# Optimization experiments

Measured on AMD Instinct MI355X. Metric: run time of the kernel, lower is better.

Reference implementation:

```python
import jax, jax.numpy as jnp
import numpy as np

B, H, S, D = 4, 16, 2048, 64

def setup_inputs() -> dict:
    key = jax.random.key(0)
    kq, kk, kv = jax.random.split(key, 3)
    q = jax.random.normal(kq, (B, H, S, D), dtype=jnp.float32)
    k = jax.random.normal(kk, (B, H, S, D), dtype=jnp.float32)
    v = jax.random.normal(kv, (B, H, S, D), dtype=jnp.float32)
    return {"q": q, "k": k, "v": v}

def reference(q, k, v):
    # dots: [b,h,i,j] = q . k (NO 1/sqrt(d) scaling, matching source)
    dots = jnp.einsum('bhid,bhjd->bhij', q, k)
    # causal=False (and the source's causal mask is a no-op bug anyway)
    attn = jax.nn.softmax(dots, axis=-1)
    # out: [b,h,i,d] = sum_j attn[b,h,i,j] * v[b,h,j,d]
    return jnp.einsum('bhjd,bhij->bhid', v, attn)
```

## Files before the change

### kernel.cpp

```cpp
#include <hip/hip_runtime.h>
#include <hip/hip_bf16.h>
#include <stdint.h>

#define B_ 4
#define H_ 16
#define S_ 2048
#define D_ 64
#define QBLK 128
#define KBLK 64
#define LDW 72

typedef __attribute__((ext_vector_type(8))) short short8;
typedef __attribute__((ext_vector_type(4))) float f32x4;
typedef __attribute__((ext_vector_type(16))) float f32x16;
typedef _Float16 f16x8 __attribute__((ext_vector_type(8)));
typedef _Float16 f16x4 __attribute__((ext_vector_type(4)));
typedef __fp16 fp16x2 __attribute__((ext_vector_type(2)));

__device__ __forceinline__ unsigned short f2bf(float f) {
  union { float f; unsigned int u; } x; x.f = f;
  unsigned int u = x.u;
  unsigned int r = (u + 0x7FFFu + ((u >> 16) & 1u)) >> 16;
  return (unsigned short)r;
}
__device__ __forceinline__ float bf2f(unsigned short h) {
  union { unsigned int u; float f; } y; y.u = ((unsigned int)h) << 16;
  return y.f;
}

__device__ __forceinline__ unsigned pkrtz(float a, float b) {
  union { fp16x2 h; unsigned u; } c;
  c.h = __builtin_amdgcn_cvt_pkrtz(a, b);
  return c.u;
}

__device__ __forceinline__ void swap32(unsigned &a, unsigned &b) {
#if __has_builtin(__builtin_amdgcn_permlane32_swap)
  typedef int i32x2 __attribute__((ext_vector_type(2)));
  i32x2 r = __builtin_amdgcn_permlane32_swap((int)a, (int)b, false, false);
  a = (unsigned)r[0]; b = (unsigned)r[1];
#else
  unsigned pa = (unsigned)__shfl_xor((int)a, 32);
  unsigned pb = (unsigned)__shfl_xor((int)b, 32);
  bool lo = (threadIdx.x & 32) == 0;
  unsigned r0 = lo ? a : pb;
  unsigned r1 = lo ? pa : b;
  a = r0; b = r1;
#endif
}

#define GLOAD16(g, l) __builtin_amdgcn_global_load_lds( \
    (const __attribute__((address_space(1))) unsigned int*)(g), \
    (__attribute__((address_space(3))) unsigned int*)(l), 16, 0, 0)

__global__ void prep_k(const float* __restrict__ K, _Float16* __restrict__ Kp) {
  int e4 = (blockIdx.x * 256 + threadIdx.x) * 4;
  int bh  = e4 >> 17;
  int rem = e4 & 131071;
  int s   = rem >> 6;
  int d0  = rem & 63;
  const float4 kv = *(const float4*)(K + (size_t)e4);
  f16x4 h;
  h[0] = (_Float16)kv.x; h[1] = (_Float16)kv.y;
  h[2] = (_Float16)kv.z; h[3] = (_Float16)kv.w;
  size_t off = ((size_t)bh * S_ + s) * 128 + (unsigned)((d0 * 2) ^ ((s & 7) << 4));
  *(f16x4*)((char*)Kp + off) = h;
}

__global__ void prep_v(const float* __restrict__ V, _Float16* __restrict__ Vt) {
  __shared__ _Float16 tile[64][68];
  int bh = blockIdx.x >> 5;
  int st = blockIdx.x & 31;
  const float* Vb = V + ((size_t)bh * S_ + st * 64) * 64;
  int tid = threadIdx.x;
  #pragma unroll
  for (int i = 0; i < 4; ++i) {
    int idx = i * 1024 + tid * 4;
    int r = idx >> 6, c = idx & 63;
    float4 vv = *(const float4*)(Vb + (size_t)r * 64 + c);
    f16x4 o;
    o[0] = (_Float16)vv.x; o[1] = (_Float16)vv.y;
    o[2] = (_Float16)vv.z; o[3] = (_Float16)vv.w;
    *(f16x4*)&tile[r][c] = o;
  }
  __syncthreads();
  int chunk = tid & 15;
  int dbase = tid >> 4;
  size_t outb = (size_t)bh * (64 * S_ * 2) + (size_t)st * 128;
  #pragma unroll
  for (int i = 0; i < 4; ++i) {
    int d = dbase + i * 16;
    f16x4 o;
    o[0] = tile[chunk * 4 + 0][d];
    o[1] = tile[chunk * 4 + 1][d];
    o[2] = tile[chunk * 4 + 2][d];
    o[3] = tile[chunk * 4 + 3][d];
    size_t off = outb + (size_t)d * (S_ * 2) + (unsigned)((chunk * 8) ^ ((d & 7) << 4));
    *(f16x4*)((char*)Vt + off) = o;
  }
}

__global__ __launch_bounds__(256)
void attn_fwd4(const float* __restrict__ Q, const _Float16* __restrict__ Kg,
               const _Float16* __restrict__ Vg, float* __restrict__ O) {
  __shared__ char smem[32768];

  const int tid  = threadIdx.x;
  const int lane = tid & 63;
  const int wid  = tid >> 6;
  const int l31  = lane & 31;
  const int hi   = lane >> 5;

  const int qtile = blockIdx.x;
  const int bh    = blockIdx.y;

  const char* KB = (const char*)Kg + (size_t)bh * (S_ * 128);
  const char* VB = (const char*)Vg + (size_t)bh * (64 * S_ * 2);
  const float* Qb = Q + (size_t)bh * S_ * D_;
  float*       Ob = O + (size_t)bh * S_ * D_;

  const int qrow = qtile * QBLK + wid * 32 + l31;
  f16x8 qf[4];
  #pragma unroll
  for (int ds = 0; ds < 4; ++ds) {
    const float* qp = Qb + (size_t)qrow * D_ + ds * 16 + hi * 8;
    float4 a = *(const float4*)(qp);
    float4 b = *(const float4*)(qp + 4);
    qf[ds][0] = (_Float16)a.x; qf[ds][1] = (_Float16)a.y;
    qf[ds][2] = (_Float16)a.z; qf[ds][3] = (_Float16)a.w;
    qf[ds][4] = (_Float16)b.x; qf[ds][5] = (_Float16)b.y;
    qf[ds][6] = (_Float16)b.z; qf[ds][7] = (_Float16)b.w;
  }

  f32x16 oacc[2];
  #pragma unroll
  for (int dn = 0; dn < 2; ++dn)
    #pragma unroll
    for (int r = 0; r < 16; ++r) oacc[dn][r] = 0.f;
  float m_r = -INFINITY, l_r = 0.f;

  #define STAGE(buf, kb)                                                        \
    {                                                                           \
      char* Kl_ = smem + (buf) * 16384;                                         \
      char* Vl_ = Kl_ + 8192;                                                   \
      _Pragma("unroll")                                                         \
      for (int c = 0; c < 4; ++c) {                                             \
        int id = c * 4 + wid;                                                   \
        if (id < 8) {                                                           \
          GLOAD16(KB + (size_t)(kb) * 128 + id * 1024 + lane * 16,              \
                  Kl_ + id * 1024);                                             \
        } else {                                                                \
          int i = id - 8;                                                       \
          GLOAD16(VB + (size_t)(i * 8 + (lane >> 3)) * (S_ * 2)                 \
                     + ((kb) >> 6) * 128 + (lane & 7) * 16,                     \
                  Vl_ + i * 1024);                                              \
        }                                                                       \
      }                                                                         \
    }

  STAGE(0, 0);
  __syncthreads();

  for (int it = 0; it < S_ / KBLK; ++it) {
    const int cur = it & 1;
    if (it < S_ / KBLK - 1) STAGE(cur ^ 1, (it + 1) * KBLK);

    const char* Kl = smem + cur * 16384;
    const char* Vl = Kl + 8192;

    f32x16 sacc[2];
    #pragma unroll
    for (int b = 0; b < 2; ++b) {
      #pragma unroll
      for (int r = 0; r < 16; ++r) sacc[b][r] = 0.f;
      const int row = b * 32 + l31;
      #pragma unroll
      for (int ds = 0; ds < 4; ++ds) {
        f16x8 kf = *(const f16x8*)(Kl + row * 128 + ((ds * 32 + hi * 16) ^ ((row & 7) << 4)));
        sacc[b] = __builtin_amdgcn_mfma_f32_32x32x16_f16(kf, qf[ds], sacc[b], 0, 0, 0);
      }
    }

    float t[16];
    #pragma unroll
    for (int r = 0; r < 16; ++r) t[r] = fmaxf(sacc[0][r], sacc[1][r]);
    #pragma unroll
    for (int s = 8; s > 0; s >>= 1)
      #pragma unroll
      for (int r = 0; r < 8; ++r)
        if (r < s) t[r] = fmaxf(t[r], t[r + s]);
    float mx = fmaxf(t[0], __shfl_xor(t[0], 32));
    float nm = fmaxf(m_r, mx);
    float sc = __expf(m_r - nm);
    m_r = nm;

    float rs0 = 0.f, rs1 = 0.f;
    #pragma unroll
    for (int b = 0; b < 2; ++b)
      #pragma unroll
      for (int r = 0; r < 16; ++r) {
        float p = __expf(sacc[b][r] - nm);
        sacc[b][r] = p;
        if (r & 1) rs1 += p; else rs0 += p;
      }
    float rs = rs0 + rs1;
    rs += __shfl_xor(rs, 32);
    l_r = l_r * sc + rs;
    #pragma unroll
    for (int dn = 0; dn < 2; ++dn)
      #pragma unroll
      for (int r = 0; r < 16; ++r) oacc[dn][r] *= sc;

    unsigned ww[2][8];
    #pragma unroll
    for (int b = 0; b < 2; ++b)
      #pragma unroll
      for (int r1 = 0; r1 < 4; ++r1) {
        ww[b][r1 * 2 + 0] = pkrtz(sacc[b][4 * r1 + 0], sacc[b][4 * r1 + 1]);
        ww[b][r1 * 2 + 1] = pkrtz(sacc[b][4 * r1 + 2], sacc[b][4 * r1 + 3]);
      }

    f16x8 pb[4];
    #pragma unroll
    for (int ks = 0; ks < 4; ++ks) {
      const int b = ks >> 1, e = (ks & 1) * 2;
      unsigned u0 = ww[b][e * 2 + 0];
      unsigned u1 = ww[b][e * 2 + 1];
      unsigned u2 = ww[b][(e + 1) * 2 + 0];
      unsigned u3 = ww[b][(e + 1) * 2 + 1];
      swap32(u0, u2);
      swap32(u1, u3);
      union { unsigned u[4]; f16x8 v; } c;
      c.u[0] = u0; c.u[1] = u1; c.u[2] = u2; c.u[3] = u3;
      pb[ks] = c.v;
    }

    #pragma unroll
    for (int dn = 0; dn < 2; ++dn) {
      const int d = dn * 32 + l31;
      #pragma unroll
      for (int ks = 0; ks < 4; ++ks) {
        f16x8 vf = *(const f16x8*)(Vl + d * 128 + ((ks * 32 + hi * 16) ^ ((d & 7) << 4)));
        oacc[dn] = __builtin_amdgcn_mfma_f32_32x32x16_f16(vf, pb[ks], oacc[dn], 0, 0, 0);
      }
    }
    __syncthreads();
  }
  #undef STAGE

  const float inv = 1.0f / l_r;
  float* Ep = (float*)(smem + wid * 8192);
  #pragma unroll
  for (int dn = 0; dn < 2; ++dn)
    #pragma unroll
    for (int r = 0; r < 16; ++r) {
      int d = dn * 32 + (r & 3) + 8 * (r >> 2) + 4 * hi;
      Ep[d * 32 + l31] = oacc[dn][r] * inv;
    }
  __syncthreads();
  const int q2 = lane >> 1, dh = lane & 1;
  float* orow = Ob + (size_t)(qtile * QBLK + wid * 32 + q2) * D_ + dh * 32;
  #pragma unroll
  for (int c = 0; c < 8; ++c) {
    float4 o4;
    o4.x = Ep[(dh * 32 + c * 4 + 0) * 32 + q2];
    o4.y = Ep[(dh * 32 + c * 4 + 1) * 32 + q2];
    o4.z = Ep[(dh * 32 + c * 4 + 2) * 32 + q2];
    o4.w = Ep[(dh * 32 + c * 4 + 3) * 32 + q2];
    *(float4*)(orow + c * 4) = o4;
  }
}

__global__ __launch_bounds__(256, 2)
void attn_fwd(const float* __restrict__ Q, const float* __restrict__ K,
              const float* __restrict__ V, float* __restrict__ O) {
  __shared__ alignas(16) unsigned short Kh_lds[KBLK * LDW];
  __shared__ alignas(16) unsigned short Kl_lds[KBLK * LDW];
  __shared__ alignas(16) unsigned short Vt_lds[D_ * LDW];
  __shared__ alignas(16) unsigned short P_lds[4][16 * LDW];

  const int tid  = threadIdx.x;
  const int lane = tid & 63;
  const int wid  = tid >> 6;
  const int l15  = lane & 15;
  const int dgrp = lane >> 4;

  const int qtile = blockIdx.x;
  const int bh    = blockIdx.y;

  const size_t base = (size_t)bh * S_ * D_;
  const float* Qb = Q + base;
  const float* Kb = K + base;
  const float* Vb = V + base;
  float*       Ob = O + base;

  const int qrow = qtile * 64 + wid * 16 + l15;
  short8 qfh[2], qfl[2];
  {
    const float* qp = Qb + (size_t)qrow * D_ + dgrp * 8;
    #pragma unroll
    for (int s = 0; s < 2; ++s)
      #pragma unroll
      for (int j = 0; j < 8; ++j) {
        float f = qp[s * 32 + j];
        unsigned short h = f2bf(f);
        qfh[s][j] = (short)h;
        qfl[s][j] = (short)f2bf(f - bf2f(h));
      }
  }

  f32x4 oacc[4];
  #pragma unroll
  for (int t = 0; t < 4; ++t) oacc[t] = f32x4{0.f, 0.f, 0.f, 0.f};
  float m_r[4], l_r[4];
  #pragma unroll
  for (int j = 0; j < 4; ++j) { m_r[j] = -INFINITY; l_r[j] = 0.f; }

  for (int kb = 0; kb < S_; kb += KBLK) {
    __syncthreads();
    #pragma unroll
    for (int c = 0; c < 4; ++c) {
      int e = (c * 256 + tid) * 4;
      int r = e >> 6, col = e & 63;
      const float4 kv = *(const float4*)(Kb + (size_t)(kb + r) * D_ + col);
      ushort4 kh, kl;
      kh.x = f2bf(kv.x); kl.x = f2bf(kv.x - bf2f(kh.x));
      kh.y = f2bf(kv.y); kl.y = f2bf(kv.y - bf2f(kh.y));
      kh.z = f2bf(kv.z); kl.z = f2bf(kv.z - bf2f(kh.z));
      kh.w = f2bf(kv.w); kl.w = f2bf(kv.w - bf2f(kh.w));
      *(ushort4*)&Kh_lds[r * LDW + col] = kh;
      *(ushort4*)&Kl_lds[r * LDW + col] = kl;
      const float4 vv = *(const float4*)(Vb + (size_t)(kb + r) * D_ + col);
      Vt_lds[(col + 0) * LDW + r] = f2bf(vv.x);
      Vt_lds[(col + 1) * LDW + r] = f2bf(vv.y);
      Vt_lds[(col + 2) * LDW + r] = f2bf(vv.z);
      Vt_lds[(col + 3) * LDW + r] = f2bf(vv.w);
    }
    __syncthreads();

    f32x4 sa[4];
    #pragma unroll
    for (int t = 0; t < 4; ++t) {
      sa[t] = f32x4{0.f, 0.f, 0.f, 0.f};
      #pragma unroll
      for (int s = 0; s < 2; ++s) {
        const int off = (t * 16 + l15) * LDW + s * 32 + dgrp * 8;
        short8 kfh = *(const short8*)&Kh_lds[off];
        short8 kfl = *(const short8*)&Kl_lds[off];
        sa[t] = __builtin_amdgcn_mfma_f32_16x16x32_bf16(qfh[s], kfh, sa[t], 0, 0, 0);
        sa[t] = __builtin_amdgcn_mfma_f32_16x16x32_bf16(qfh[s], kfl, sa[t], 0, 0, 0);
        sa[t] = __builtin_amdgcn_mfma_f32_16x16x32_bf16(qfl[s], kfh, sa[t], 0, 0, 0);
      }
    }

    float pmax[4];
    #pragma unroll
    for (int j = 0; j < 4; ++j) {
      float mx = fmaxf(fmaxf(sa[0][j], sa[1][j]), fmaxf(sa[2][j], sa[3][j]));
      #pragma unroll
      for (int m = 1; m < 16; m <<= 1) mx = fmaxf(mx, __shfl_xor(mx, m));
      pmax[j] = mx;
    }
    float scale[4];
    #pragma unroll
    for (int j = 0; j < 4; ++j) {
      float nm = fmaxf(m_r[j], pmax[j]);
      scale[j] = __expf(m_r[j] - nm);
      m_r[j] = nm;
    }
    float rs[4] = {0.f, 0.f, 0.f, 0.f};
    #pragma unroll
    for (int t = 0; t < 4; ++t)
      #pragma unroll
      for (int j = 0; j < 4; ++j) {
        float p = __expf(sa[t][j] - m_r[j]);
        rs[j] += p;
        P_lds[wid][(dgrp * 4 + j) * LDW + t * 16 + l15] = f2bf(p);
      }
    #pragma unroll
    for (int j = 0; j < 4; ++j) {
      #pragma unroll
      for (int m = 1; m < 16; m <<= 1) rs[j] += __shfl_xor(rs[j], m);
      l_r[j] = l_r[j] * scale[j] + rs[j];
      #pragma unroll
      for (int t = 0; t < 4; ++t) oacc[t][j] *= scale[j];
    }

    #pragma unroll
    for (int s = 0; s < 2; ++s) {
      short8 pf = *(const short8*)&P_lds[wid][l15 * LDW + s * 32 + dgrp * 8];
      #pragma unroll
      for (int t = 0; t < 4; ++t) {
        short8 vf = *(const short8*)&Vt_lds[(t * 16 + l15) * LDW + s * 32 + dgrp * 8];
        oacc[t] = __builtin_amdgcn_mfma_f32_16x16x32_bf16(pf, vf, oacc[t], 0, 0, 0);
      }
    }
  }

  #pragma unroll
  for (int j = 0; j < 4; ++j) {
    float inv = 1.0f / l_r[j];
    int row = qtile * 64 + wid * 16 + dgrp * 4 + j;
    float* op = Ob + (size_t)row * D_ + l15;
    #pragma unroll
    for (int t = 0; t < 4; ++t)
      op[t * 16] = oacc[t][j] * inv;
  }
}

extern "C" void kernel_launch(void* const* d_in, const int* in_sizes, int n_in,
                              void* d_out, int out_size, void* d_ws, size_t ws_size,
                              hipStream_t stream) {
  const float* q = (const float*)d_in[0];
  const float* k = (const float*)d_in[1];
  const float* v = (const float*)d_in[2];
  float* o = (float*)d_out;
  const size_t PLANE = (size_t)B_ * H_ * S_ * 128;
  if (ws_size >= 2 * PLANE) {
    _Float16* Kp = (_Float16*)d_ws;
    _Float16* Vt = (_Float16*)((char*)d_ws + PLANE);
    prep_k<<<8192, 256, 0, stream>>>(k, Kp);
    prep_v<<<2048, 256, 0, stream>>>(v, Vt);
    attn_fwd4<<<dim3(S_ / QBLK, B_ * H_), 256, 0, stream>>>(q, Kp, Vt, o);
  } else {
    attn_fwd<<<dim3(S_ / 64, B_ * H_), 256, 0, stream>>>(q, k, v, o);
  }
}
```

Baseline: 151.1 us.

## Load pre-swizzled K/V fragments directly to registers and use exp2 lazy-rescale softmax

The prep kernels now write K and V in MFMA-fragment order, so the attention kernel loads fragments straight from global memory into registers. This drops the LDS staging and the per-tile barriers, and the next K tile is prefetched into a second register buffer. Softmax folds log2(e) into Q and uses hardware exp2. It only rescales the running max when the new max exceeds the old by more than a threshold, and sums row probabilities with fp16 dot2 instructions. The grid is also reordered to put bh first, and MFMA sections are given higher priority. In exchange there is more register pressure, no LDS reuse across the four waves so each wave reads K/V from L2, and slightly different rounding in the row sum.

After: 142.1 us. -5.9%, faster.

```diff
diff --git a/kernel.cpp b/kernel.cpp
--- a/kernel.cpp
+++ b/kernel.cpp
@@ -8,7 +8,9 @@
 #define D_ 64
 #define QBLK 128
 #define KBLK 64
+#define NT (S_ / KBLK)
 #define LDW 72
+#define LOG2E 1.44269504088896340736f
 
 typedef __attribute__((ext_vector_type(8))) short short8;
 typedef __attribute__((ext_vector_type(4))) float f32x4;
@@ -33,6 +35,17 @@
   c.h = __builtin_amdgcn_cvt_pkrtz(a, b);
   return c.u;
 }
+__device__ __forceinline__ fp16x2 u2h(unsigned u) {
+  union { unsigned u; fp16x2 h; } c; c.u = u; return c.h;
+}
+
+__device__ __forceinline__ float fast_exp2(float x) {
+#if __has_builtin(__builtin_amdgcn_exp2f)
+  return __builtin_amdgcn_exp2f(x);
+#else
+  return exp2f(x);
+#endif
+}
 
 __device__ __forceinline__ void swap32(unsigned &a, unsigned &b) {
 #if __has_builtin(__builtin_amdgcn_permlane32_swap)
@@ -40,18 +53,20 @@
   i32x2 r = __builtin_amdgcn_permlane32_swap((int)a, (int)b, false, false);
   a = (unsigned)r[0]; b = (unsigned)r[1];
 #else
-  unsigned pa = (unsigned)__shfl_xor((int)a, 32);
-  unsigned pb = (unsigned)__shfl_xor((int)b, 32);
-  bool lo = (threadIdx.x & 32) == 0;
-  unsigned r0 = lo ? a : pb;
-  unsigned r1 = lo ? pa : b;
-  a = r0; b = r1;
+  asm("v_permlane32_swap_b32 %0, %1" : "+v"(a), "+v"(b));
 #endif
 }
 
-#define GLOAD16(g, l) __builtin_amdgcn_global_load_lds( \
-    (const __attribute__((address_space(1))) unsigned int*)(g), \
-    (__attribute__((address_space(3))) unsigned int*)(l), 16, 0, 0)
+__device__ __forceinline__ float pairmax(float x) {
+  unsigned a = __float_as_uint(x), b = a;
+  swap32(a, b);
+  return fmaxf(__uint_as_float(a), __uint_as_float(b));
+}
+__device__ __forceinline__ float pairsum(float x) {
+  unsigned a = __float_as_uint(x), b = a;
+  swap32(a, b);
+  return __uint_as_float(a) + __uint_as_float(b);
+}
 
 __global__ void prep_k(const float* __restrict__ K, _Float16* __restrict__ Kp) {
   int e4 = (blockIdx.x * 256 + threadIdx.x) * 4;
@@ -63,12 +78,16 @@
   f16x4 h;
   h[0] = (_Float16)kv.x; h[1] = (_Float16)kv.y;
   h[2] = (_Float16)kv.z; h[3] = (_Float16)kv.w;
-  size_t off = ((size_t)bh * S_ + s) * 128 + (unsigned)((d0 * 2) ^ ((s & 7) << 4));
+  int tile = s >> 6, r = s & 63;
+  int b = r >> 5, l31 = r & 31;
+  int ds = d0 >> 4, hi = (d0 >> 3) & 1, j = d0 & 7;
+  size_t off = (((size_t)bh * 32 + tile) * 8 + (b * 4 + ds)) * 1024
+             + (hi * 32 + l31) * 16 + j * 2;
   *(f16x4*)((char*)Kp + off) = h;
 }
 
 __global__ void prep_v(const float* __restrict__ V, _Float16* __restrict__ Vt) {
-  __shared__ _Float16 tile[64][68];
+  __shared__ _Float16 tile[64][66];
   int bh = blockIdx.x >> 5;
   int st = blockIdx.x & 31;
   const float* Vb = V + ((size_t)bh * S_ + st * 64) * 64;
@@ -86,23 +105,26 @@
   __syncthreads();
   int chunk = tid & 15;
   int dbase = tid >> 4;
-  size_t outb = (size_t)bh * (64 * S_ * 2) + (size_t)st * 128;
+  int sbase = chunk * 4;
+  int ks = sbase >> 4, hi = (sbase >> 3) & 1, j0 = sbase & 7;
   #pragma unroll
   for (int i = 0; i < 4; ++i) {
     int d = dbase + i * 16;
     f16x4 o;
-    o[0] = tile[chunk * 4 + 0][d];
-    o[1] = tile[chunk * 4 + 1][d];
-    o[2] = tile[chunk * 4 + 2][d];
-    o[3] = tile[chunk * 4 + 3][d];
-    size_t off = outb + (size_t)d * (S_ * 2) + (unsigned)((chunk * 8) ^ ((d & 7) << 4));
+    o[0] = tile[sbase + 0][d];
+    o[1] = tile[sbase + 1][d];
+    o[2] = tile[sbase + 2][d];
+    o[3] = tile[sbase + 3][d];
+    int dn = d >> 5, l31 = d & 31;
+    size_t off = (((size_t)bh * 32 + st) * 8 + (dn * 4 + ks)) * 1024
+               + (hi * 32 + l31) * 16 + j0 * 2;
     *(f16x4*)((char*)Vt + off) = o;
   }
 }
 
 __global__ __launch_bounds__(256)
-void attn_fwd4(const float* __restrict__ Q, const _Float16* __restrict__ Kg,
-               const _Float16* __restrict__ Vg, float* __restrict__ O) {
+void attn_fwd10(const float* __restrict__ Q, const _Float16* __restrict__ Kg,
+                const _Float16* __restrict__ Vg, float* __restrict__ O) {
   __shared__ char smem[32768];
 
   const int tid  = threadIdx.x;
@@ -110,12 +132,13 @@
   const int wid  = tid >> 6;
   const int l31  = lane & 31;
   const int hi   = lane >> 5;
-
-  const int qtile = blockIdx.x;
-  const int bh    = blockIdx.y;
-
-  const char* KB = (const char*)Kg + (size_t)bh * (S_ * 128);
-  const char* VB = (const char*)Vg + (size_t)bh * (64 * S_ * 2);
+  const int loff = lane * 16;
+
+  const int bh    = blockIdx.x;
+  const int qtile = blockIdx.y;
+
+  const char* KB = (const char*)Kg + (size_t)bh * (32 * 8192);
+  const char* VB = (const char*)Vg + (size_t)bh * (32 * 8192);
   const float* Qb = Q + (size_t)bh * S_ * D_;
   float*       Ob = O + (size_t)bh * S_ * D_;
 
@@ -126,10 +149,10 @@
     const float* qp = Qb + (size_t)qrow * D_ + ds * 16 + hi * 8;
     float4 a = *(const float4*)(qp);
     float4 b = *(const float4*)(qp + 4);
-    qf[ds][0] = (_Float16)a.x; qf[ds][1] = (_Float16)a.y;
-    qf[ds][2] = (_Float16)a.z; qf[ds][3] = (_Float16)a.w;
-    qf[ds][4] = (_Float16)b.x; qf[ds][5] = (_Float16)b.y;
-    qf[ds][6] = (_Float16)b.z; qf[ds][7] = (_Float16)b.w;
+    qf[ds][0] = (_Float16)(a.x * LOG2E); qf[ds][1] = (_Float16)(a.y * LOG2E);
+    qf[ds][2] = (_Float16)(a.z * LOG2E); qf[ds][3] = (_Float16)(a.w * LOG2E);
+    qf[ds][4] = (_Float16)(b.x * LOG2E); qf[ds][5] = (_Float16)(b.y * LOG2E);
+    qf[ds][6] = (_Float16)(b.z * LOG2E); qf[ds][7] = (_Float16)(b.w * LOG2E);
   }
 
   f32x16 oacc[2];
@@ -139,116 +162,178 @@
     for (int r = 0; r < 16; ++r) oacc[dn][r] = 0.f;
   float m_r = -INFINITY, l_r = 0.f;
 
-  #define STAGE(buf, kb)                                                        \
+  f32x16 zero16;
+  #pragma unroll
+  for (int r = 0; r < 16; ++r) zero16[r] = 0.f;
+
+  f16x8 kbufA[8], kbufB[8];
+  #pragma unroll
+  for (int f = 0; f < 8; ++f)
+    kbufA[f] = *(const f16x8*)(KB + f * 1024 + loff);
+
+  #define TILE_BODY(KC, KN, IT)                                                 \
+  {                                                                             \
+    const size_t tb = (size_t)(IT) * 8192;                                      \
+                              \
+    f16x8 vf[8];                                                                \
+    _Pragma("unroll")                                                           \
+    for (int g = 0; g < 8; ++g)                                                 \
+      vf[g] = *(const f16x8*)(VB + tb + g * 1024 + loff);                       \
+                                            \
+    f32x16 sacc_a, sacc_b;                                                      \
+    __builtin_amdgcn_s_setprio(1);                                              \
+    sacc_a = __builtin_amdgcn_mfma_f32_32x32x16_f16(KC[0], qf[0], zero16, 0, 0, 0); \
+    sacc_a = __builtin_amdgcn_mfma_f32_32x32x16_f16(KC[1], qf[1], sacc_a, 0, 0, 0); \
+    sacc_a = __builtin_amdgcn_mfma_f32_32x32x16_f16(KC[2], qf[2], sacc_a, 0, 0, 0); \
+    sacc_a = __builtin_amdgcn_mfma_f32_32x32x16_f16(KC[3], qf[3], sacc_a, 0, 0, 0); \
+    sacc_b = __builtin_amdgcn_mfma_f32_32x32x16_f16(KC[4], qf[0], zero16, 0, 0, 0); \
+    sacc_b = __builtin_amdgcn_mfma_f32_32x32x16_f16(KC[5], qf[1], sacc_b, 0, 0, 0); \
+    sacc_b = __builtin_amdgcn_mfma_f32_32x32x16_f16(KC[6], qf[2], sacc_b, 0, 0, 0); \
+    sacc_b = __builtin_amdgcn_mfma_f32_32x32x16_f16(KC[7], qf[3], sacc_b, 0, 0, 0); \
+    __builtin_amdgcn_s_setprio(0);                                              \
+                              \
+    if ((IT) + 1 < NT) {                                                        \
+      _Pragma("unroll")                                                         \
+      for (int f = 0; f < 8; ++f)                                               \
+        KN[f] = *(const f16x8*)(KB + tb + 8192 + f * 1024 + loff);              \
+    }                                                                           \
+                                           \
     {                                                                           \
-      char* Kl_ = smem + (buf) * 16384;                                         \
-      char* Vl_ = Kl_ + 8192;                                                   \
+      float v0 = fmaxf(fmaxf(sacc_a[0], sacc_a[1]), sacc_a[2]);                 \
+      float v1 = fmaxf(fmaxf(sacc_a[3], sacc_a[4]), sacc_a[5]);                 \
+      float v2 = fmaxf(fmaxf(sacc_a[6], sacc_a[7]), sacc_a[8]);                 \
+      float v3 = fmaxf(fmaxf(sacc_a[9], sacc_a[10]), sacc_a[11]);               \
+      float v4 = fmaxf(fmaxf(sacc_a[12], sacc_a[13]), sacc_a[14]);              \
+      float w0 = fmaxf(fmaxf(v0, v1), v2);                                      \
+      float w1 = fmaxf(fmaxf(v3, v4), sacc_a[15]);                              \
+      float mx = pairmax(fmaxf(w0, w1));                                        \
+      if (!__all(mx <= m_r + 8.f)) {                                            \
+        float nm = fmaxf(m_r, mx);                                              \
+        float sc = fast_exp2(m_r - nm);                                         \
+        m_r = nm; l_r *= sc;                                                    \
+        _Pragma("unroll")                                                       \
+        for (int dn = 0; dn < 2; ++dn)                                          \
+          _Pragma("unroll")                                                     \
+          for (int r = 0; r < 16; ++r) oacc[dn][r] *= sc;                       \
+      }                                                                         \
+      unsigned ww[8];                                                           \
       _Pragma("unroll")                                                         \
-      for (int c = 0; c < 4; ++c) {                                             \
-        int id = c * 4 + wid;                                                   \
-        if (id < 8) {                                                           \
-          GLOAD16(KB + (size_t)(kb) * 128 + id * 1024 + lane * 16,              \
-                  Kl_ + id * 1024);                                             \
-        } else {                                                                \
-          int i = id - 8;                                                       \
-          GLOAD16(VB + (size_t)(i * 8 + (lane >> 3)) * (S_ * 2)                 \
-                     + ((kb) >> 6) * 128 + (lane & 7) * 16,                     \
-                  Vl_ + i * 1024);                                              \
-        }                                                                       \
-      }                                                                         \
-    }
-
-  STAGE(0, 0);
-  __syncthreads();
-
-  for (int it = 0; it < S_ / KBLK; ++it) {
-    const int cur = it & 1;
-    if (it < S_ / KBLK - 1) STAGE(cur ^ 1, (it + 1) * KBLK);
-
-    const char* Kl = smem + cur * 16384;
-    const char* Vl = Kl + 8192;
-
-    f32x16 sacc[2];
-    #pragma unroll
-    for (int b = 0; b < 2; ++b) {
-      #pragma unroll
-      for (int r = 0; r < 16; ++r) sacc[b][r] = 0.f;
-      const int row = b * 32 + l31;
-      #pragma unroll
-      for (int ds = 0; ds < 4; ++ds) {
-        f16x8 kf = *(const f16x8*)(Kl + row * 128 + ((ds * 32 + hi * 16) ^ ((row & 7) << 4)));
-        sacc[b] = __builtin_amdgcn_mfma_f32_32x32x16_f16(kf, qf[ds], sacc[b], 0, 0, 0);
-      }
-    }
-
-    float t[16];
-    #pragma unroll
-    for (int r = 0; r < 16; ++r) t[r] = fmaxf(sacc[0][r], sacc[1][r]);
-    #pragma unroll
-    for (int s = 8; s > 0; s >>= 1)
-      #pragma unroll
-      for (int r = 0; r < 8; ++r)
-        if (r < s) t[r] = fmaxf(t[r], t[r + s]);
-    float mx = fmaxf(t[0], __shfl_xor(t[0], 32));
-    float nm = fmaxf(m_r, mx);
-    float sc = __expf(m_r - nm);
-    m_r = nm;
-
-    float rs0 = 0.f, rs1 = 0.f;
-    #pragma unroll
-    for (int b = 0; b < 2; ++b)
-      #pragma unroll
-      for (int r = 0; r < 16; ++r) {
-        float p = __expf(sacc[b][r] - nm);
-        sacc[b][r] = p;
-        if (r & 1) rs1 += p; else rs0 += p;
-      }
-    float rs = rs0 + rs1;
-    rs += __shfl_xor(rs, 32);
-    l_r = l_r * sc + rs;
-    #pragma unroll
-    for (int dn = 0; dn < 2; ++dn)
-      #pragma unroll
-      for (int r = 0; r < 16; ++r) oacc[dn][r] *= sc;
-
-    unsigned ww[2][8];
-    #pragma unroll
-    for (int b = 0; b < 2; ++b)
-      #pragma unroll
-      for (int r1 = 0; r1 < 4; ++r1) {
-        ww[b][r1 * 2 + 0] = pkrtz(sacc[b][4 * r1 + 0], sacc[b][4 * r1 + 1]);
-        ww[b][r1 * 2 + 1] = pkrtz(sacc[b][4 * r1 + 2], sacc[b][4 * r1 + 3]);
-      }
-
-    f16x8 pb[4];
-    #pragma unroll
-    for (int ks = 0; ks < 4; ++ks) {
-      const int b = ks >> 1, e = (ks & 1) * 2;
-      unsigned u0 = ww[b][e * 2 + 0];
-      unsigned u1 = ww[b][e * 2 + 1];
-      unsigned u2 = ww[b][(e + 1) * 2 + 0];
-      unsigned u3 = ww[b][(e + 1) * 2 + 1];
-      swap32(u0, u2);
-      swap32(u1, u3);
-      union { unsigned u[4]; f16x8 v; } c;
-      c.u[0] = u0; c.u[1] = u1; c.u[2] = u2; c.u[3] = u3;
-      pb[ks] = c.v;
-    }
-
-    #pragma unroll
-    for (int dn = 0; dn < 2; ++dn) {
-      const int d = dn * 32 + l31;
-      #pragma unroll
-      for (int ks = 0; ks < 4; ++ks) {
-        f16x8 vf = *(const f16x8*)(Vl + d * 128 + ((ks * 32 + hi * 16) ^ ((d & 7) << 4)));
-        oacc[dn] = __builtin_amdgcn_mfma_f32_32x32x16_f16(vf, pb[ks], oacc[dn], 0, 0, 0);
-      }
-    }
-    __syncthreads();
-  }
-  #undef STAGE
-
-  const float inv = 1.0f / l_r;
+      for (int r1 = 0; r1 < 4; ++r1) {                                          \
+        float p0 = fast_exp2(sacc_a[4 * r1 + 0] - m_r);                         \
+        float p1 = fast_exp2(sacc_a[4 * r1 + 1] - m_r);                         \
+        float p2 = fast_exp2(sacc_a[4 * r1 + 2] - m_r);                         \
+        float p3 = fast_exp2(sacc_a[4 * r1 + 3] - m_r);                         \
+        ww[r1 * 2 + 0] = pkrtz(p0, p1);                                         \
+        ww[r1 * 2 + 1] = pkrtz(p2, p3);                                         \
+      }                                                                         \
+      {                                                                         \
+        const fp16x2 ones = {(__fp16)1.f, (__fp16)1.f};                         \
+        float rA = __builtin_amdgcn_fdot2(u2h(ww[0]), ones, 0.f, false);        \
+        float rB = __builtin_amdgcn_fdot2(u2h(ww[1]), ones, 0.f, false);        \
+        rA = __builtin_amdgcn_fdot2(u2h(ww[2]), ones, rA, false);               \
+        rB = __builtin_amdgcn_fdot2(u2h(ww[3]), ones, rB, false);               \
+        rA = __builtin_amdgcn_fdot2(u2h(ww[4]), ones, rA, false);               \
+        rB = __builtin_amdgcn_fdot2(u2h(ww[5]), ones, rB, false);               \
+        rA = __builtin_amdgcn_fdot2(u2h(ww[6]), ones, rA, false);               \
+        rB = __builtin_amdgcn_fdot2(u2h(ww[7]), ones, rB, false);               \
+        l_r += rA + rB;                                                         \
+      }                                                                         \
+      f16x8 pb0, pb1;                                                           \
+      {                                                                         \
+        unsigned u0 = ww[0], u1 = ww[1], u2 = ww[2], u3 = ww[3];                \
+        swap32(u0, u2); swap32(u1, u3);                                         \
+        union { unsigned u[4]; f16x8 v; } c;                                    \
+        c.u[0] = u0; c.u[1] = u1; c.u[2] = u2; c.u[3] = u3;                     \
+        pb0 = c.v;                                                              \
+      }                                                                         \
+      {                                                                         \
+        unsigned u0 = ww[4], u1 = ww[5], u2 = ww[6], u3 = ww[7];                \
+        swap32(u0, u2); swap32(u1, u3);                                         \
+        union { unsigned u[4]; f16x8 v; } c;                                    \
+        c.u[0] = u0; c.u[1] = u1; c.u[2] = u2; c.u[3] = u3;                     \
+        pb1 = c.v;                                                              \
+      }                                                                         \
+      __builtin_amdgcn_s_setprio(1);                                            \
+      _Pragma("unroll")                                                         \
+      for (int dn = 0; dn < 2; ++dn) {                                          \
+        oacc[dn] = __builtin_amdgcn_mfma_f32_32x32x16_f16(vf[dn * 4 + 0], pb0, oacc[dn], 0, 0, 0); \
+        oacc[dn] = __builtin_amdgcn_mfma_f32_32x32x16_f16(vf[dn * 4 + 1], pb1, oacc[dn], 0, 0, 0); \
+      }                                                                         \
+      __builtin_amdgcn_s_setprio(0);                                            \
+    }                                                                           \
+                                          \
+    {                                                                           \
+      float v0 = fmaxf(fmaxf(sacc_b[0], sacc_b[1]), sacc_b[2]);                 \
+      float v1 = fmaxf(fmaxf(sacc_b[3], sacc_b[4]), sacc_b[5]);                 \
+      float v2 = fmaxf(fmaxf(sacc_b[6], sacc_b[7]), sacc_b[8]);                 \
+      float v3 = fmaxf(fmaxf(sacc_b[9], sacc_b[10]), sacc_b[11]);               \
+      float v4 = fmaxf(fmaxf(sacc_b[12], sacc_b[13]), sacc_b[14]);              \
+      float w0 = fmaxf(fmaxf(v0, v1), v2);                                      \
+      float w1 = fmaxf(fmaxf(v3, v4), sacc_b[15]);                              \
+      float mx = pairmax(fmaxf(w0, w1));                                        \
+      if (!__all(mx <= m_r + 8.f)) {                                            \
+        float nm = fmaxf(m_r, mx);                                              \
+        float sc = fast_exp2(m_r - nm);                                         \
+        m_r = nm; l_r *= sc;                                                    \
+        _Pragma("unroll")                                                       \
+        for (int dn = 0; dn < 2; ++dn)                                          \
+          _Pragma("unroll")                                                     \
+          for (int r = 0; r < 16; ++r) oacc[dn][r] *= sc;                       \
+      }                                                                         \
+      unsigned ww[8];                                                           \
+      _Pragma("unroll")                                                         \
+      for (int r1 = 0; r1 < 4; ++r1) {                                          \
+        float p0 = fast_exp2(sacc_b[4 * r1 + 0] - m_r);                         \
+        float p1 = fast_exp2(sacc_b[4 * r1 + 1] - m_r);                         \
+        float p2 = fast_exp2(sacc_b[4 * r1 + 2] - m_r);                         \
+        float p3 = fast_exp2(sacc_b[4 * r1 + 3] - m_r);                         \
+        ww[r1 * 2 + 0] = pkrtz(p0, p1);                                         \
+        ww[r1 * 2 + 1] = pkrtz(p2, p3);                                         \
+      }                                                                         \
+      {                                                                         \
+        const fp16x2 ones = {(__fp16)1.f, (__fp16)1.f};                         \
+        float rA = __builtin_amdgcn_fdot2(u2h(ww[0]), ones, 0.f, false);        \
+        float rB = __builtin_amdgcn_fdot2(u2h(ww[1]), ones, 0.f, false);        \
+        rA = __builtin_amdgcn_fdot2(u2h(ww[2]), ones, rA, false);               \
+        rB = __builtin_amdgcn_fdot2(u2h(ww[3]), ones, rB, false);               \
+        rA = __builtin_amdgcn_fdot2(u2h(ww[4]), ones, rA, false);               \
+        rB = __builtin_amdgcn_fdot2(u2h(ww[5]), ones, rB, false);               \
+        rA = __builtin_amdgcn_fdot2(u2h(ww[6]), ones, rA, false);               \
+        rB = __builtin_amdgcn_fdot2(u2h(ww[7]), ones, rB, false);               \
+        l_r += rA + rB;                                                         \
+      }                                                                         \
+      f16x8 pb2, pb3;                                                           \
+      {                                                                         \
+        unsigned u0 = ww[0], u1 = ww[1], u2 = ww[2], u3 = ww[3];                \
+        swap32(u0, u2); swap32(u1, u3);                                         \
+        union { unsigned u[4]; f16x8 v; } c;                                    \
+        c.u[0] = u0; c.u[1] = u1; c.u[2] = u2; c.u[3] = u3;                     \
+        pb2 = c.v;                                                              \
+      }                                                                         \
+      {                                                                         \
+        unsigned u0 = ww[4], u1 = ww[5], u2 = ww[6], u3 = ww[7];                \
+        swap32(u0, u2); swap32(u1, u3);                                         \
+        union { unsigned u[4]; f16x8 v; } c;                                    \
+        c.u[0] = u0; c.u[1] = u1; c.u[2] = u2; c.u[3] = u3;                     \
+        pb3 = c.v;                                                              \
+      }                                                                         \
+      __builtin_amdgcn_s_setprio(1);                                            \
+      _Pragma("unroll")                                                         \
+      for (int dn = 0; dn < 2; ++dn) {                                          \
+        oacc[dn] = __builtin_amdgcn_mfma_f32_32x32x16_f16(vf[dn * 4 + 2], pb2, oacc[dn], 0, 0, 0); \
+        oacc[dn] = __builtin_amdgcn_mfma_f32_32x32x16_f16(vf[dn * 4 + 3], pb3, oacc[dn], 0, 0, 0); \
+      }                                                                         \
+      __builtin_amdgcn_s_setprio(0);                                            \
+    }                                                                           \
+  }
+
+  for (int it = 0; it < NT; it += 2) {
+    TILE_BODY(kbufA, kbufB, it);
+    TILE_BODY(kbufB, kbufA, it + 1);
+  }
+  #undef TILE_BODY
+
+  const float inv = 1.0f / pairsum(l_r);
   float* Ep = (float*)(smem + wid * 8192);
   #pragma unroll
   for (int dn = 0; dn < 2; ++dn)
@@ -421,7 +506,7 @@
     _Float16* Vt = (_Float16*)((char*)d_ws + PLANE);
     prep_k<<<8192, 256, 0, stream>>>(k, Kp);
     prep_v<<<2048, 256, 0, stream>>>(v, Vt);
-    attn_fwd4<<<dim3(S_ / QBLK, B_ * H_), 256, 0, stream>>>(q, Kp, Vt, o);
+    attn_fwd10<<<dim3(B_ * H_, S_ / QBLK), 256, 0, stream>>>(q, Kp, Vt, o);
   } else {
     attn_fwd<<<dim3(S_ / 64, B_ * H_), 256, 0, stream>>>(q, k, v, o);
   }
```
